# Kernel optimization log

Hardware: AMD Instinct MI355X
Metric: run time of the kernel (lower is better)

The kernel has to match this reference:

```python
import jax, jax.numpy as jnp
import numpy as np

N = 50000  # num nodes


def _spmm(edge_index, edge_w, x):
    # sparse [N,N] @ dense [N,d] via gather + segment-sum
    row, col = edge_index[0], edge_index[1]
    msgs = edge_w[:, None] * x[col]                      # [E, d]
    return jax.ops.segment_sum(msgs, row, num_segments=N)


def setup_inputs() -> dict:
    key = jax.random.key(0)
    k1, k2, k3, k4, k5 = jax.random.split(key, 5)
    E1, E2, d = 800000, 1600000, 128
    x = jax.random.normal(k1, (N, d), dtype=jnp.float32)
    edge_index1 = jax.random.randint(k2, (2, E1), 0, N, dtype=jnp.int64)
    edge_w1 = jax.random.uniform(k3, (E1,), dtype=jnp.float32)
    edge_index2 = jax.random.randint(k4, (2, E2), 0, N, dtype=jnp.int64)
    edge_w2 = jax.random.uniform(k5, (E2,), dtype=jnp.float32)
    return {"x": x, "edge_index1": edge_index1, "edge_w1": edge_w1,
            "edge_index2": edge_index2, "edge_w2": edge_w2}


def reference(x, edge_index1, edge_w1, edge_index2, edge_w2):
    x1 = _spmm(edge_index1, edge_w1, x)   # adj_t  @ x  -> [N, d]
    x2 = _spmm(edge_index2, edge_w2, x)   # adj_t2 @ x  -> [N, d]
    return jnp.concatenate([x1, x2], axis=1)  # [N, 2d]
```

## Files before the change

kernel.cpp:

```cpp
#include <hip/hip_runtime.h>
#include <hip/hip_cooperative_groups.h>


#define N_NODES 50000
#define D 128
#define OUT_STRIDE 256

#define BSHIFT 6
#define BROWS 64
#define NBUCK ((N_NODES + BROWS - 1) >> BSHIFT)
#define BBITS 10
#define CHUNK 5120
#define NTHR 1024
#define NWAVE 16
#define WSEG (CHUNK / NWAVE)
#define SITERS (WSEG / 64)
#define ACAP 4096
#define GRID 512

#define SM_SIZE 50688
#define SO_REC  0
#define SO_RL   20480
#define SO_HWC  25600
#define SO_WSUM 50624
#define AO_RECS 0
#define AO_OUTB 16384
#define AO_RL   32768
#define AO_CROW 36864
#define AO_CUR  37120
#define AO_RST  37376
#define AO_TOT  37632

typedef float vf2 __attribute__((ext_vector_type(2)));

static inline size_t align256(size_t x) { return (x + 255) & ~(size_t)255; }

__device__ __forceinline__ unsigned f32_to_bf16_bits(float f) {
    unsigned u = __float_as_uint(f);
    return (u + 0x7fffu + ((u >> 16) & 1u)) >> 16;
}

template<int BITS>
__device__ __forceinline__ unsigned long long wave_match(int v, bool valid) {
    unsigned long long m = __ballot(valid ? 1 : 0);
    #pragma unroll
    for (int k = 0; k < BITS; ++k) {
        unsigned long long vb = __ballot((v >> k) & 1);
        m &= ((v >> k) & 1) ? vb : ~vb;
    }
    return m;
}


__device__ __forceinline__ void dev_cvt(const float* __restrict__ x,
                                        unsigned* __restrict__ xb, int n4) {
    for (long long i = (long long)blockIdx.x * NTHR + threadIdx.x; i < n4;
         i += (long long)gridDim.x * NTHR) {
        float4 v = ((const float4*)x)[i];
        unsigned a = f32_to_bf16_bits(v.x);
        unsigned b = f32_to_bf16_bits(v.y);
        unsigned c = f32_to_bf16_bits(v.z);
        unsigned d = f32_to_bf16_bits(v.w);
        ((uint2*)xb)[i] = make_uint2(a | (b << 16), c | (d << 16));
    }
}


__device__ void dev_scatter(int cid,
        const int* __restrict__ ei1, const float* __restrict__ w1, int E1, int nch1,
        const int* __restrict__ ei2, const float* __restrict__ w2, int E2,
        unsigned* __restrict__ irec, unsigned char* __restrict__ irl,
        int* __restrict__ ends, char* sm) {
    unsigned*       stage_rec = (unsigned*)(sm + SO_REC);
    unsigned char*  stage_rl  = (unsigned char*)(sm + SO_RL);
    unsigned short* hwc       = (unsigned short*)(sm + SO_HWC);
    int*            wsum      = (int*)(sm + SO_WSUM);

    int g = (cid < nch1) ? 0 : 1;
    int chunk = g ? cid - nch1 : cid;
    const int*   ei = g ? ei2 : ei1;
    const float* w  = g ? w2  : w1;
    int E           = g ? E2  : E1;
    int e0  = chunk * CHUNK;
    int cnt = min(CHUNK, E - e0);

    int t = threadIdx.x, lane = t & 63, wid = t >> 6;
    unsigned long long below = (1ull << lane) - 1ull;
    for (int i = t; i < (NWAVE * NBUCK) / 2; i += NTHR) ((int*)hwc)[i] = 0;
    __syncthreads();

    int s0 = wid * WSEG, s1 = min(cnt, s0 + WSEG);
    unsigned meta[SITERS];
    unsigned recs[SITERS];
    #pragma unroll
    for (int k = 0; k < SITERS; ++k) {
        int i = s0 + k * 64 + lane;
        bool v = (i < s1);
        int row = v ? ei[e0 + i] : 0;
        int col = v ? ei[E + e0 + i] : 0;
        float wv = v ? w[e0 + i] : 0.f;
        int bb = row >> BSHIFT;
        unsigned long long m = wave_match<BBITS>(bb, v);
        unsigned rank = (unsigned)__popcll(m & below);
        unsigned base = hwc[wid * NBUCK + bb];
        if (v && (m & below) == 0)
            hwc[wid * NBUCK + bb] = (unsigned short)(base + (unsigned)__popcll(m));
        meta[k] = (unsigned)bb | ((unsigned)(row & 63) << 10) | ((base + rank) << 16);
        recs[k] = (unsigned)col | (f32_to_bf16_bits(wv) << 16);
    }
    __syncthreads();
    {
        int tot = 0;
        if (t < NBUCK) {
            #pragma unroll
            for (int q = 0; q < NWAVE; ++q) tot += hwc[q * NBUCK + t];
        }
        int s = tot;
        #pragma unroll
        for (int d2 = 1; d2 < 64; d2 <<= 1) { int u = __shfl_up(s, d2, 64); if (lane >= d2) s += u; }
        if (lane == 63) wsum[wid] = s;
        __syncthreads();
        int add = 0;
        #pragma unroll
        for (int k = 0; k < NWAVE; ++k) if (k < wid) add += wsum[k];
        s += add;
        if (t < NBUCK) {
            int a = s - tot;
            #pragma unroll
            for (int q = 0; q < NWAVE; ++q) {
                int hq = hwc[q * NBUCK + t];
                hwc[q * NBUCK + t] = (unsigned short)a;
                a += hq;
            }
            ends[(size_t)cid * NBUCK + t] = a;
        }
    }
    __syncthreads();
    #pragma unroll
    for (int k = 0; k < SITERS; ++k) {
        int i = s0 + k * 64 + lane;
        if (i < s1) {
            unsigned mk = meta[k];
            unsigned bb = mk & 1023u;
            unsigned pos = (mk >> 16) + hwc[wid * NBUCK + bb];
            stage_rec[pos] = recs[k];
            stage_rl[pos] = (unsigned char)((mk >> 10) & 63u);
        }
    }
    __syncthreads();
    for (int i = t; i < cnt; i += NTHR) {
        irec[(size_t)cid * CHUNK + i] = stage_rec[i];
        irl[(size_t)cid * CHUNK + i]  = stage_rl[i];
    }
}


__device__ __forceinline__ void fma_rec(unsigned p, unsigned rec, float& ax, float& ay) {
    float w = __int_as_float((int)(rec & 0xffff0000u));
    ax += w * __int_as_float((int)(p << 16));
    ay += w * __int_as_float((int)(p & 0xffff0000u));
}

__device__ void dev_accum(int b, int g, int nch1, int nch2,
        const unsigned* __restrict__ irec, const unsigned char* __restrict__ irl,
        const int* __restrict__ ends, const unsigned* __restrict__ xb,
        float* __restrict__ out, char* sm) {
    unsigned*      arecs = (unsigned*)(sm + AO_RECS);
    unsigned*      aoutb = (unsigned*)(sm + AO_OUTB);
    unsigned char* arl   = (unsigned char*)(sm + AO_RL);
    int* crow   = (int*)(sm + AO_CROW);
    int* cur    = (int*)(sm + AO_CUR);
    int* rstart = (int*)(sm + AO_RST);
    int* total  = (int*)(sm + AO_TOT);

    int c0 = g ? nch1 : 0;
    int nc = g ? nch2 : nch1;
    int t = threadIdx.x, lane = t & 63, wid = t >> 6;
    if (t < BROWS) crow[t] = 0;
    if (t == 0) *total = 0;
    __syncthreads();
    for (int ci = t; ci < nc; ci += NTHR) {
        const int* ep = ends + (size_t)(c0 + ci) * NBUCK;
        int s = b ? ep[b - 1] : 0;
        int e = ep[b];
        int n = e - s;
        if (!n) continue;
        int dst = atomicAdd(total, n);
        const unsigned* sr = irec + (size_t)(c0 + ci) * CHUNK + s;
        const unsigned char* sl = irl + (size_t)(c0 + ci) * CHUNK + s;
        int k = 0;
        for (; k + 2 <= n; k += 2) {
            unsigned r0 = sr[k], r1 = sr[k + 1];
            unsigned char l0 = sl[k], l1 = sl[k + 1];
            int p0 = dst + k, p1 = dst + k + 1;
            if (p0 < ACAP) { arl[p0] = l0; arecs[p0] = r0; atomicAdd(&crow[l0], 1); }
            if (p1 < ACAP) { arl[p1] = l1; arecs[p1] = r1; atomicAdd(&crow[l1], 1); }
        }
        if (k < n) {
            unsigned r0 = sr[k];
            unsigned char l0 = sl[k];
            int p0 = dst + k;
            if (p0 < ACAP) { arl[p0] = l0; arecs[p0] = r0; atomicAdd(&crow[l0], 1); }
        }
    }
    __syncthreads();
    int cnt = min(*total, ACAP);
    if (wid == 0) {
        int v = crow[lane], s = v;
        #pragma unroll
        for (int d2 = 1; d2 < 64; d2 <<= 1) { int u = __shfl_up(s, d2, 64); if (lane >= d2) s += u; }
        cur[lane] = s - v;
        rstart[lane] = s - v;
    }
    __syncthreads();
    for (int i = t; i < cnt; i += NTHR) {
        int pos = atomicAdd(&cur[arl[i]], 1);
        aoutb[pos] = arecs[i];
    }
    __syncthreads();
    for (int r = wid * 4; r < wid * 4 + 4; ++r) {
        int grow = (b << BSHIFT) + r;
        if (grow >= N_NODES) break;
        int rs = rstart[r], re = cur[r];
        float ax = 0.f, ay = 0.f;
        int j = rs;
        for (; j + 4 <= re; j += 4) {
            unsigned c0r = aoutb[j];
            unsigned c1r = aoutb[j + 1];
            unsigned c2r = aoutb[j + 2];
            unsigned c3r = aoutb[j + 3];
            unsigned p0 = xb[(size_t)(c0r & 0xffffu) * 64 + lane];
            unsigned p1 = xb[(size_t)(c1r & 0xffffu) * 64 + lane];
            unsigned p2 = xb[(size_t)(c2r & 0xffffu) * 64 + lane];
            unsigned p3 = xb[(size_t)(c3r & 0xffffu) * 64 + lane];
            fma_rec(p0, c0r, ax, ay);
            fma_rec(p1, c1r, ax, ay);
            fma_rec(p2, c2r, ax, ay);
            fma_rec(p3, c3r, ax, ay);
        }
        for (; j < re; ++j) {
            unsigned cr = aoutb[j];
            unsigned p = xb[(size_t)(cr & 0xffffu) * 64 + lane];
            fma_rec(p, cr, ax, ay);
        }
        vf2 rv; rv.x = ax; rv.y = ay;
        vf2* o = (vf2*)(out + (size_t)grow * OUT_STRIDE + g * D);
        __builtin_nontemporal_store(rv, o + lane);
    }
}


__global__ void __launch_bounds__(NTHR, 8) k_fused(
        const int* ei1, const float* w1, int E1, int nch1,
        const int* ei2, const float* w2, int E2, int nch2, int ncht,
        unsigned* irec, unsigned char* irl, int* ends,
        const float* x, unsigned* xb, int n4, float* out) {
    __shared__ alignas(16) char sm[SM_SIZE];
    dev_cvt(x, xb, n4);
    if ((int)blockIdx.x < ncht)
        dev_scatter(blockIdx.x, ei1, w1, E1, nch1, ei2, w2, E2, irec, irl, ends, sm);
    cooperative_groups::this_grid().sync();
    for (int task = blockIdx.x; task < 2 * NBUCK; task += gridDim.x) {
        int g = task >= NBUCK;
        int b = g ? task - NBUCK : task;
        __syncthreads();
        dev_accum(b, g, nch1, nch2, irec, irl, ends, xb, out, sm);
    }
}


__global__ void __launch_bounds__(NTHR, 8) k_prep(
        const int* ei1, const float* w1, int E1, int nch1,
        const int* ei2, const float* w2, int E2, int ncht,
        unsigned* irec, unsigned char* irl, int* ends,
        const float* x, unsigned* xb, int n4) {
    __shared__ alignas(16) char sm[SM_SIZE];
    dev_cvt(x, xb, n4);
    if ((int)blockIdx.x < ncht)
        dev_scatter(blockIdx.x, ei1, w1, E1, nch1, ei2, w2, E2, irec, irl, ends, sm);
}

__global__ void __launch_bounds__(NTHR, 8) k_accum(
        const unsigned* irec, const unsigned char* irl, const int* ends,
        const unsigned* xb, float* out, int nch1, int nch2) {
    __shared__ alignas(16) char sm[AO_TOT + 16];
    int task = blockIdx.x;
    int g = task >= NBUCK;
    int b = g ? task - NBUCK : task;
    dev_accum(b, g, nch1, nch2, irec, irl, ends, xb, out, sm);
}


__global__ void spmm_scatter(const float* __restrict__ x,
                             const int* __restrict__ ei,
                             const float* __restrict__ w,
                             float* __restrict__ out,
                             int E, int col_off) {
    long long gid = (long long)blockIdx.x * blockDim.x + threadIdx.x;
    int e    = (int)(gid >> 5);
    int lane = (int)(gid & 31);
    if (e >= E) return;
    int row  = ei[e];
    int col  = ei[E + e];
    float wv = w[e];
    const float4* xv = (const float4*)(x + (size_t)col * D);
    float4 v = xv[lane];
    float* o = out + (size_t)row * OUT_STRIDE + col_off + lane * 4;
    atomicAdd(o + 0, wv * v.x);
    atomicAdd(o + 1, wv * v.y);
    atomicAdd(o + 2, wv * v.z);
    atomicAdd(o + 3, wv * v.w);
}

extern "C" void kernel_launch(void* const* d_in, const int* in_sizes, int n_in,
                              void* d_out, int out_size, void* d_ws, size_t ws_size,
                              hipStream_t stream) {
    const int*   ei1_p = (const int*)d_in[1];
    const float* w1_p  = (const float*)d_in[2];
    const int*   ei2_p = (const int*)d_in[3];
    const float* w2_p  = (const float*)d_in[4];
    const float* x_p   = (const float*)d_in[0];
    float* out_p = (float*)d_out;

    int E1 = in_sizes[1] / 2;
    int E2 = in_sizes[3] / 2;
    const int block = 256;

    int nch1 = (E1 + CHUNK - 1) / CHUNK;
    int nch2 = (E2 + CHUNK - 1) / CHUNK;
    int ncht = nch1 + nch2;
    int n4   = N_NODES * 32;

    size_t rec_b  = align256((size_t)ncht * CHUNK * sizeof(unsigned));
    size_t rl_b   = align256((size_t)ncht * CHUNK);
    size_t ends_b = align256((size_t)ncht * NBUCK * sizeof(int));
    size_t xb_b   = align256((size_t)N_NODES * 64 * sizeof(unsigned));
    size_t o_rec  = 0;
    size_t o_rl   = o_rec + rec_b;
    size_t o_ends = o_rl + rl_b;
    size_t o_xb   = o_ends + ends_b;
    size_t needed = o_xb + xb_b;

    bool shape_ok = (ncht <= GRID) && (nch1 <= NTHR) && (nch2 <= NTHR);

    if (ws_size < needed || !shape_ok) {
        (void)hipMemsetAsync(d_out, 0, (size_t)out_size * sizeof(float), stream);
        long long th1 = (long long)E1 * 32;
        spmm_scatter<<<(int)((th1 + block - 1) / block), block, 0, stream>>>(
            x_p, ei1_p, w1_p, out_p, E1, 0);
        long long th2 = (long long)E2 * 32;
        spmm_scatter<<<(int)((th2 + block - 1) / block), block, 0, stream>>>(
            x_p, ei2_p, w2_p, out_p, E2, D);
        return;
    }

    char* ws = (char*)d_ws;
    unsigned*      irec = (unsigned*)(ws + o_rec);
    unsigned char* irl  = (unsigned char*)(ws + o_rl);
    int*           ends = (int*)(ws + o_ends);
    unsigned*      xb   = (unsigned*)(ws + o_xb);

    int occ = 0;
    hipError_t qe = hipOccupancyMaxActiveBlocksPerMultiprocessor(&occ, k_fused, NTHR, 0);
    if (qe == hipSuccess && occ >= 2) {
        void* ka[] = { (void*)&ei1_p, (void*)&w1_p, (void*)&E1, (void*)&nch1,
                       (void*)&ei2_p, (void*)&w2_p, (void*)&E2, (void*)&nch2,
                       (void*)&ncht, (void*)&irec, (void*)&irl, (void*)&ends,
                       (void*)&x_p, (void*)&xb, (void*)&n4, (void*)&out_p };
        (void)hipLaunchCooperativeKernel((const void*)k_fused, dim3(GRID), dim3(NTHR),
                                         ka, 0, stream);
        return;
    }

    k_prep<<<GRID, NTHR, 0, stream>>>(ei1_p, w1_p, E1, nch1, ei2_p, w2_p, E2,
                                      ncht, irec, irl, ends, x_p, xb, n4);
    k_accum<<<2 * NBUCK, NTHR, 0, stream>>>(irec, irl, ends, xb, out_p, nch1, nch2);
}
```

Baseline: 228.1 us.

## Replace cooperative fused kernel with two launches and smaller blocks

Removes the cooperative single-kernel path with its grid-wide barrier and always runs a separate prep kernel and accumulate kernel. Block size drops from 1024 to 512 threads, the chunk from 5120 to 4096 edges, and the accumulate capacity from 4096 to 3072. The bucket scan now has each thread handle two buckets so fewer threads cover all buckets. This trades the grid-sync cost for an extra launch boundary. The smaller per-bucket record capacity raises the chance that dense buckets overflow it.

```diff
diff --git a/kernel.cpp b/kernel.cpp
--- a/kernel.cpp
+++ b/kernel.cpp
@@ -1,5 +1,4 @@
 #include <hip/hip_runtime.h>
-#include <hip/hip_cooperative_groups.h>
 
 
 #define N_NODES 50000
@@ -10,26 +9,12 @@
 #define BROWS 64
 #define NBUCK ((N_NODES + BROWS - 1) >> BSHIFT)
 #define BBITS 10
-#define CHUNK 5120
-#define NTHR 1024
-#define NWAVE 16
+#define CHUNK 4096
+#define NTHR 512
+#define NWAVE 8
 #define WSEG (CHUNK / NWAVE)
 #define SITERS (WSEG / 64)
-#define ACAP 4096
-#define GRID 512
-
-#define SM_SIZE 50688
-#define SO_REC  0
-#define SO_RL   20480
-#define SO_HWC  25600
-#define SO_WSUM 50624
-#define AO_RECS 0
-#define AO_OUTB 16384
-#define AO_RL   32768
-#define AO_CROW 36864
-#define AO_CUR  37120
-#define AO_RST  37376
-#define AO_TOT  37632
+#define ACAP 3072
 
 typedef float vf2 __attribute__((ext_vector_type(2)));
 
@@ -52,9 +37,20 @@
 }
 
 
-__device__ __forceinline__ void dev_cvt(const float* __restrict__ x,
-                                        unsigned* __restrict__ xb, int n4) {
-    for (long long i = (long long)blockIdx.x * NTHR + threadIdx.x; i < n4;
+__global__ void __launch_bounds__(NTHR) k_prep(
+        const int* __restrict__ ei1, const float* __restrict__ w1, int E1, int nch1,
+        const int* __restrict__ ei2, const float* __restrict__ w2, int E2, int ncht,
+        unsigned* __restrict__ irec, unsigned char* __restrict__ irl,
+        int* __restrict__ ends,
+        const float* __restrict__ x, unsigned* __restrict__ xb, int n4) {
+    __shared__ unsigned stage_rec[CHUNK];
+    __shared__ unsigned char stage_rl[CHUNK];
+    __shared__ unsigned short hwc[NWAVE][NBUCK];
+    __shared__ int wsum[NWAVE];
+
+    int t = threadIdx.x, lane = t & 63, wid = t >> 6;
+
+    for (long long i = (long long)blockIdx.x * NTHR + t; i < n4;
          i += (long long)gridDim.x * NTHR) {
         float4 v = ((const float4*)x)[i];
         unsigned a = f32_to_bf16_bits(v.x);
@@ -63,19 +59,9 @@
         unsigned d = f32_to_bf16_bits(v.w);
         ((uint2*)xb)[i] = make_uint2(a | (b << 16), c | (d << 16));
     }
-}
-
-
-__device__ void dev_scatter(int cid,
-        const int* __restrict__ ei1, const float* __restrict__ w1, int E1, int nch1,
-        const int* __restrict__ ei2, const float* __restrict__ w2, int E2,
-        unsigned* __restrict__ irec, unsigned char* __restrict__ irl,
-        int* __restrict__ ends, char* sm) {
-    unsigned*       stage_rec = (unsigned*)(sm + SO_REC);
-    unsigned char*  stage_rl  = (unsigned char*)(sm + SO_RL);
-    unsigned short* hwc       = (unsigned short*)(sm + SO_HWC);
-    int*            wsum      = (int*)(sm + SO_WSUM);
-
+
+    int cid = blockIdx.x;
+    if (cid >= ncht) return;
     int g = (cid < nch1) ? 0 : 1;
     int chunk = g ? cid - nch1 : cid;
     const int*   ei = g ? ei2 : ei1;
@@ -84,7 +70,6 @@
     int e0  = chunk * CHUNK;
     int cnt = min(CHUNK, E - e0);
 
-    int t = threadIdx.x, lane = t & 63, wid = t >> 6;
     unsigned long long below = (1ull << lane) - 1ull;
     for (int i = t; i < (NWAVE * NBUCK) / 2; i += NTHR) ((int*)hwc)[i] = 0;
     __syncthreads();
@@ -102,20 +87,26 @@
         int bb = row >> BSHIFT;
         unsigned long long m = wave_match<BBITS>(bb, v);
         unsigned rank = (unsigned)__popcll(m & below);
-        unsigned base = hwc[wid * NBUCK + bb];
+        unsigned base = hwc[wid][bb];
         if (v && (m & below) == 0)
-            hwc[wid * NBUCK + bb] = (unsigned short)(base + (unsigned)__popcll(m));
+            hwc[wid][bb] = (unsigned short)(base + (unsigned)__popcll(m));
         meta[k] = (unsigned)bb | ((unsigned)(row & 63) << 10) | ((base + rank) << 16);
         recs[k] = (unsigned)col | (f32_to_bf16_bits(wv) << 16);
     }
     __syncthreads();
     {
-        int tot = 0;
-        if (t < NBUCK) {
+        int b0 = 2 * t, b1 = b0 + 1;
+        int h0[NWAVE], h1[NWAVE];
+        int t0 = 0, t1 = 0;
+        if (b0 < NBUCK) {
             #pragma unroll
-            for (int q = 0; q < NWAVE; ++q) tot += hwc[q * NBUCK + t];
-        }
-        int s = tot;
+            for (int q = 0; q < NWAVE; ++q) { h0[q] = hwc[q][b0]; t0 += h0[q]; }
+        }
+        if (b1 < NBUCK) {
+            #pragma unroll
+            for (int q = 0; q < NWAVE; ++q) { h1[q] = hwc[q][b1]; t1 += h1[q]; }
+        }
+        int p = t0 + t1, s = p;
         #pragma unroll
         for (int d2 = 1; d2 < 64; d2 <<= 1) { int u = __shfl_up(s, d2, 64); if (lane >= d2) s += u; }
         if (lane == 63) wsum[wid] = s;
@@ -124,15 +115,18 @@
         #pragma unroll
         for (int k = 0; k < NWAVE; ++k) if (k < wid) add += wsum[k];
         s += add;
-        if (t < NBUCK) {
-            int a = s - tot;
+        int excl = s - p;
+        if (b0 < NBUCK) {
+            int a = excl;
             #pragma unroll
-            for (int q = 0; q < NWAVE; ++q) {
-                int hq = hwc[q * NBUCK + t];
-                hwc[q * NBUCK + t] = (unsigned short)a;
-                a += hq;
-            }
-            ends[(size_t)cid * NBUCK + t] = a;
+            for (int q = 0; q < NWAVE; ++q) { int h = h0[q]; hwc[q][b0] = (unsigned short)a; a += h; }
+            ends[(size_t)cid * NBUCK + b0] = a;
+        }
+        if (b1 < NBUCK) {
+            int a = excl + t0;
+            #pragma unroll
+            for (int q = 0; q < NWAVE; ++q) { int h = h1[q]; hwc[q][b1] = (unsigned short)a; a += h; }
+            ends[(size_t)cid * NBUCK + b1] = a;
         }
     }
     __syncthreads();
@@ -142,7 +136,7 @@
         if (i < s1) {
             unsigned mk = meta[k];
             unsigned bb = mk & 1023u;
-            unsigned pos = (mk >> 16) + hwc[wid * NBUCK + bb];
+            unsigned pos = (mk >> 16) + hwc[wid][bb];
             stage_rec[pos] = recs[k];
             stage_rl[pos] = (unsigned char)((mk >> 10) & 63u);
         }
@@ -161,23 +155,24 @@
     ay += w * __int_as_float((int)(p & 0xffff0000u));
 }
 
-__device__ void dev_accum(int b, int g, int nch1, int nch2,
+__global__ void __launch_bounds__(NTHR) k_accum(
         const unsigned* __restrict__ irec, const unsigned char* __restrict__ irl,
         const int* __restrict__ ends, const unsigned* __restrict__ xb,
-        float* __restrict__ out, char* sm) {
-    unsigned*      arecs = (unsigned*)(sm + AO_RECS);
-    unsigned*      aoutb = (unsigned*)(sm + AO_OUTB);
-    unsigned char* arl   = (unsigned char*)(sm + AO_RL);
-    int* crow   = (int*)(sm + AO_CROW);
-    int* cur    = (int*)(sm + AO_CUR);
-    int* rstart = (int*)(sm + AO_RST);
-    int* total  = (int*)(sm + AO_TOT);
-
+        float* __restrict__ out, int nch1, int nch2) {
+    int task = blockIdx.x;
+    int g = task >= NBUCK;
+    int b = g ? task - NBUCK : task;
     int c0 = g ? nch1 : 0;
     int nc = g ? nch2 : nch1;
+
+    __shared__ unsigned arecs[ACAP];
+    __shared__ unsigned aoutb[ACAP];
+    __shared__ unsigned char arl[ACAP];
+    __shared__ int crow[BROWS], cur[BROWS], rstart[BROWS];
+    __shared__ int total;
     int t = threadIdx.x, lane = t & 63, wid = t >> 6;
     if (t < BROWS) crow[t] = 0;
-    if (t == 0) *total = 0;
+    if (t == 0) total = 0;
     __syncthreads();
     for (int ci = t; ci < nc; ci += NTHR) {
         const int* ep = ends + (size_t)(c0 + ci) * NBUCK;
@@ -185,7 +180,7 @@
         int e = ep[b];
         int n = e - s;
         if (!n) continue;
-        int dst = atomicAdd(total, n);
+        int dst = atomicAdd(&total, n);
         const unsigned* sr = irec + (size_t)(c0 + ci) * CHUNK + s;
         const unsigned char* sl = irl + (size_t)(c0 + ci) * CHUNK + s;
         int k = 0;
@@ -204,7 +199,7 @@
         }
     }
     __syncthreads();
-    int cnt = min(*total, ACAP);
+    int cnt = min(total, ACAP);
     if (wid == 0) {
         int v = crow[lane], s = v;
         #pragma unroll
@@ -218,7 +213,7 @@
         aoutb[pos] = arecs[i];
     }
     __syncthreads();
-    for (int r = wid * 4; r < wid * 4 + 4; ++r) {
+    for (int r = wid * 8; r < wid * 8 + 8; ++r) {
         int grow = (b << BSHIFT) + r;
         if (grow >= N_NODES) break;
         int rs = rstart[r], re = cur[r];
@@ -247,47 +242,6 @@
         vf2* o = (vf2*)(out + (size_t)grow * OUT_STRIDE + g * D);
         __builtin_nontemporal_store(rv, o + lane);
     }
-}
-
-
-__global__ void __launch_bounds__(NTHR, 8) k_fused(
-        const int* ei1, const float* w1, int E1, int nch1,
-        const int* ei2, const float* w2, int E2, int nch2, int ncht,
-        unsigned* irec, unsigned char* irl, int* ends,
-        const float* x, unsigned* xb, int n4, float* out) {
-    __shared__ alignas(16) char sm[SM_SIZE];
-    dev_cvt(x, xb, n4);
-    if ((int)blockIdx.x < ncht)
-        dev_scatter(blockIdx.x, ei1, w1, E1, nch1, ei2, w2, E2, irec, irl, ends, sm);
-    cooperative_groups::this_grid().sync();
-    for (int task = blockIdx.x; task < 2 * NBUCK; task += gridDim.x) {
-        int g = task >= NBUCK;
-        int b = g ? task - NBUCK : task;
-        __syncthreads();
-        dev_accum(b, g, nch1, nch2, irec, irl, ends, xb, out, sm);
-    }
-}
-
-
-__global__ void __launch_bounds__(NTHR, 8) k_prep(
-        const int* ei1, const float* w1, int E1, int nch1,
-        const int* ei2, const float* w2, int E2, int ncht,
-        unsigned* irec, unsigned char* irl, int* ends,
-        const float* x, unsigned* xb, int n4) {
-    __shared__ alignas(16) char sm[SM_SIZE];
-    dev_cvt(x, xb, n4);
-    if ((int)blockIdx.x < ncht)
-        dev_scatter(blockIdx.x, ei1, w1, E1, nch1, ei2, w2, E2, irec, irl, ends, sm);
-}
-
-__global__ void __launch_bounds__(NTHR, 8) k_accum(
-        const unsigned* irec, const unsigned char* irl, const int* ends,
-        const unsigned* xb, float* out, int nch1, int nch2) {
-    __shared__ alignas(16) char sm[AO_TOT + 16];
-    int task = blockIdx.x;
-    int g = task >= NBUCK;
-    int b = g ? task - NBUCK : task;
-    dev_accum(b, g, nch1, nch2, irec, irl, ends, xb, out, sm);
 }
 
 
@@ -315,11 +269,11 @@
 extern "C" void kernel_launch(void* const* d_in, const int* in_sizes, int n_in,
                               void* d_out, int out_size, void* d_ws, size_t ws_size,
                               hipStream_t stream) {
+    const float* x_p   = (const float*)d_in[0];
     const int*   ei1_p = (const int*)d_in[1];
     const float* w1_p  = (const float*)d_in[2];
     const int*   ei2_p = (const int*)d_in[3];
     const float* w2_p  = (const float*)d_in[4];
-    const float* x_p   = (const float*)d_in[0];
     float* out_p = (float*)d_out;
 
     int E1 = in_sizes[1] / 2;
@@ -341,9 +295,7 @@
     size_t o_xb   = o_ends + ends_b;
     size_t needed = o_xb + xb_b;
 
-    bool shape_ok = (ncht <= GRID) && (nch1 <= NTHR) && (nch2 <= NTHR);
-
-    if (ws_size < needed || !shape_ok) {
+    if (ws_size < needed) {
         (void)hipMemsetAsync(d_out, 0, (size_t)out_size * sizeof(float), stream);
         long long th1 = (long long)E1 * 32;
         spmm_scatter<<<(int)((th1 + block - 1) / block), block, 0, stream>>>(
@@ -360,19 +312,9 @@
     int*           ends = (int*)(ws + o_ends);
     unsigned*      xb   = (unsigned*)(ws + o_xb);
 
-    int occ = 0;
-    hipError_t qe = hipOccupancyMaxActiveBlocksPerMultiprocessor(&occ, k_fused, NTHR, 0);
-    if (qe == hipSuccess && occ >= 2) {
-        void* ka[] = { (void*)&ei1_p, (void*)&w1_p, (void*)&E1, (void*)&nch1,
-                       (void*)&ei2_p, (void*)&w2_p, (void*)&E2, (void*)&nch2,
-                       (void*)&ncht, (void*)&irec, (void*)&irl, (void*)&ends,
-                       (void*)&x_p, (void*)&xb, (void*)&n4, (void*)&out_p };
-        (void)hipLaunchCooperativeKernel((const void*)k_fused, dim3(GRID), dim3(NTHR),
-                                         ka, 0, stream);
-        return;
-    }
-
-    k_prep<<<GRID, NTHR, 0, stream>>>(ei1_p, w1_p, E1, nch1, ei2_p, w2_p, E2,
+    k_prep<<<ncht, NTHR, 0, stream>>>(ei1_p, w1_p, E1, nch1, ei2_p, w2_p, E2,
                                       ncht, irec, irl, ends, x_p, xb, n4);
-    k_accum<<<2 * NBUCK, NTHR, 0, stream>>>(irec, irl, ends, xb, out_p, nch1, nch2);
-}
+
+    k_accum<<<2 * NBUCK, NTHR, 0, stream>>>(irec, irl, ends, xb, out_p,
+                                            nch1, nch2);
+}
```

Measured after the change: 223.8 us. Within noise of the previous version (-1.9%).
